# Performance work log

Hardware: AMD Instinct MI355X
Metric: run time of the kernel (lower is better)

The kernel has to match this reference:

```python
import jax, jax.numpy as jnp
import numpy as np

TEMP = 0.07  # temperature used as logits / 0.07 in the original


def setup_inputs() -> dict:
    key = jax.random.key(0)
    k1, k2, k3 = jax.random.split(key, 3)
    B, N, T, L, D = 8, 128, 8, 6, 256
    meta = jax.random.normal(k1, (B, N, T, L, D), dtype=jnp.float32)
    thing = jax.random.randint(k2, (B, N, T), 0, 2, dtype=jnp.int32)
    label = jax.random.randint(k3, (B, N, T), 0, 40, dtype=jnp.int32)
    return {"meta_weight_for_con": meta, "thing_gt_idx": thing, "label_tmp": label}


def _con_loss(meta, thing, label):
    # meta: [B,N,T,L,D]; thing,label: [B,N,T]
    B, N, T, L, D = meta.shape
    P = N * T
    valid = thing.reshape(B, P).astype(bool)            # [B,P] boolean gt mask
    lab = label.reshape(B, P)                           # [B,P]
    # meta_weight_b[mask] -> [K,L,D]; permute(1,0,2) -> per-layer [K,D].
    # We keep all P positions and mask instead of compacting (jit-friendly).
    w = meta.reshape(B, P, L, D).transpose(0, 2, 1, 3)  # [B,L,P,D]
    w = w / jnp.maximum(jnp.linalg.norm(w, axis=-1, keepdims=True), 1e-12)  # F.normalize
    z = jnp.einsum('blpd,blqd->blpq', w, w) / TEMP      # similarity / temp [B,L,P,P]

    same = lab[:, :, None] == lab[:, None, :]           # [B,P,P]
    vpair = valid[:, :, None] & valid[:, None, :]
    eye = jnp.eye(P, dtype=bool)
    pos_mask = same & (~eye) & vpair                    # positives: same label, not self
    neg_mask = (~same) & vpair                          # negatives: different label

    K = valid.sum(axis=1)                               # [B] ins_num_ per batch
    pos_count = pos_mask.sum(axis=-1)                   # [B,P]
    neg_count = neg_mask.sum(axis=-1)                   # [B,P]

    # --- random positive sample per (batch, layer, row), mirroring np.random.choice ---
    u = jax.random.uniform(jax.random.key(42), (B, L, P))
    r = jnp.floor(u * pos_count[:, None, :].astype(u.dtype)).astype(jnp.int32)
    r = jnp.minimum(r, jnp.maximum(pos_count - 1, 0)[:, None, :])
    ranks = jnp.cumsum(pos_mask, axis=-1) - 1           # rank of each positive in index order
    sel = pos_mask[:, None, :, :] & (ranks[:, None, :, :] == r[..., None])  # [B,L,P,P]
    zp = jnp.sum(jnp.where(sel, z, 0.0), axis=-1)       # chosen positive logit [B,L,P]
    diag = jnp.diagonal(z, axis1=-2, axis2=-1)          # self-sim fallback when no positives
    zp = jnp.where((pos_count > 0)[:, None, :], zp, diag)

    # --- last negative (original pads by repeating the last negative to K-1) ---
    iota = jnp.arange(P)
    idx_last = jnp.max(jnp.where(neg_mask, iota[None, None, :], -1), axis=-1)  # [B,P]
    idx = jnp.broadcast_to(jnp.maximum(idx_last, 0)[:, None, :, None], (B, L, P, 1))
    zl = jnp.take_along_axis(z, idx, axis=-1)[..., 0]   # [B,L,P]

    # --- stable CE with label 0: loss = lse(logits) - zp ---
    max_n = jnp.max(jnp.where(neg_mask[:, None], z, -jnp.inf), axis=-1)  # [B,L,P]
    m = jnp.maximum(zp, max_n)
    m = jnp.where(jnp.isfinite(m), m, zp)
    sum_neg = jnp.sum(jnp.where(neg_mask[:, None], jnp.exp(z - m[..., None]), 0.0), axis=-1)
    pad = jnp.maximum((K[:, None] - 1 - neg_count), 0).astype(z.dtype)   # [B,P]
    pad_term = pad[:, None, :] * jnp.where((neg_count > 0)[:, None, :], jnp.exp(zl - m), 0.0)
    loss_row = m + jnp.log(jnp.exp(zp - m) + sum_neg + pad_term) - zp    # [B,L,P]

    row_w = valid.astype(z.dtype)
    mean_per = jnp.sum(loss_row * row_w[:, None, :], axis=-1) / jnp.maximum(K, 1)[:, None].astype(z.dtype)  # [B,L]

    gate = jnp.sum((thing.sum(axis=2) > 0), axis=1) >= 2  # skip batches with <2 gt rows
    return jnp.sum(jnp.where(gate[:, None], mean_per, 0.0))


def reference(meta_weight_for_con, thing_gt_idx, label_tmp):
    return _con_loss(meta_weight_for_con, thing_gt_idx, label_tmp)
```

## Files before the change

### kernel.cpp

```cpp
#include <hip/hip_runtime.h>
#include <stdint.h>

namespace {

constexpr int Bb = 8, Ll = 6, Dd = 256, Pp = 1024;
constexpr float SCALE_Y = 14.285714285714286f * 1.4426950408889634f;
constexpr float M0y = 21.0f;
constexpr float LN2f = 0.6931471805599453f;

typedef __attribute__((ext_vector_type(4))) float floatx4;

__device__ const int PAIRS[36] = {
  0x00,0x01,0x02,0x03,0x04,0x05,0x06,0x07,
  0x11,0x12,0x13,0x14,0x15,0x16,0x17,
  0x22,0x23,0x24,0x25,0x26,0x27,
  0x33,0x34,0x35,0x36,0x37,
  0x44,0x45,0x46,0x47,
  0x55,0x56,0x57,
  0x66,0x67,
  0x77
};

__device__ __forceinline__ void async16(const void* g, void* l) {
  __builtin_amdgcn_global_load_lds(
      (const __attribute__((address_space(1))) void*)g,
      (__attribute__((address_space(3))) void*)l, 16, 0, 0);
}

__device__ __forceinline__ uint32_t rotl32(uint32_t x, int n) {
  return (x << n) | (x >> (32 - n));
}
__device__ __forceinline__ void tf_round(uint32_t& x0, uint32_t& x1, int r) {
  x0 += x1; x1 = rotl32(x1, r); x1 ^= x0;
}
__device__ void threefry2x32(uint32_t x0, uint32_t x1, uint32_t& o0, uint32_t& o1) {
  const uint32_t k0 = 0u, k1 = 42u;
  const uint32_t k2 = k0 ^ k1 ^ 0x1BD11BDAu;
  x0 += k0; x1 += k1;
  tf_round(x0,x1,13); tf_round(x0,x1,15); tf_round(x0,x1,26); tf_round(x0,x1,6);
  x0 += k1; x1 += k2 + 1u;
  tf_round(x0,x1,17); tf_round(x0,x1,29); tf_round(x0,x1,16); tf_round(x0,x1,24);
  x0 += k2; x1 += k0 + 2u;
  tf_round(x0,x1,13); tf_round(x0,x1,15); tf_round(x0,x1,26); tf_round(x0,x1,6);
  x0 += k0; x1 += k1 + 3u;
  tf_round(x0,x1,17); tf_round(x0,x1,29); tf_round(x0,x1,16); tf_round(x0,x1,24);
  x0 += k1; x1 += k2 + 4u;
  tf_round(x0,x1,13); tf_round(x0,x1,15); tf_round(x0,x1,26); tf_round(x0,x1,6);
  x0 += k2; x1 += k0 + 5u;
  o0 = x0; o1 = x1;
}
__device__ float jax_u01(uint32_t idx) {
  const uint32_t HALF = (uint32_t)(Bb * Ll * Pp / 2);
  uint32_t o0, o1, bits;
  if (idx < HALF) { threefry2x32(idx, idx + HALF, o0, o1); bits = o0; }
  else            { threefry2x32(idx - HALF, idx, o0, o1); bits = o1; }
  return __uint_as_float((bits >> 9) | 0x3f800000u) - 1.0f;
}

__device__ __forceinline__ uint32_t fp8e4m3_rne(float x) {
  uint32_t u = __float_as_uint(x);
  const uint32_t s = (u >> 24) & 0x80u;
  u &= 0x7FFFFFFFu;
  uint32_t code;
  if (u < 0x3C800000u) {
    code = (uint32_t)__float2int_rn(__uint_as_float(u) * 512.0f);
  } else {
    const uint32_t r = (u + 0x7FFFFu + ((u >> 20) & 1u)) >> 20;
    code = r - (120u << 3);
  }
  return s | code;
}
__device__ __forceinline__ float fp8e4m3_tof(uint32_t c) {
  const uint32_t e = (c >> 3) & 15u, m = c & 7u;
  float mag;
  if (e) mag = __uint_as_float(((e + 120u) << 23) | (m << 20));
  else   mag = (float)m * 0.001953125f;
  return (c & 0x80u) ? -mag : mag;
}

constexpr int NB_NORM = Bb * Pp * Ll / 4;
constexpr int NB_ROW  = Bb * Pp / 4;

__global__ void prep_k(const float* __restrict__ meta, const int* __restrict__ thing,
                       const int* __restrict__ label, uint8_t* __restrict__ wn,
                       int* __restrict__ qpos, int* __restrict__ negc,
                       int* __restrict__ qidx, int* __restrict__ Kv,
                       int* __restrict__ gatev, float* __restrict__ rowsum_g,
                       float* __restrict__ out) {
  __shared__ int sK[256], sG[256];
  const int bid = blockIdx.x, t = threadIdx.x;

  if (bid < NB_NORM) {
    const int wid = (bid * 256 + t) >> 6;
    const int lane = t & 63;
    const float4 v = *(const float4*)(meta + (size_t)wid * Dd + lane * 4);
    float ss = v.x * v.x + v.y * v.y + v.z * v.z + v.w * v.w;
    #pragma unroll
    for (int m = 32; m; m >>= 1) ss += __shfl_xor(ss, m, 64);
    const float inv = 1.0f / fmaxf(sqrtf(ss), 1e-12f);
    const int bp = wid / Ll, l = wid - bp * Ll;
    const int b = bp >> 10, p = bp & (Pp - 1);
    uint8_t* dst = wn + ((size_t)(b * Ll + l) * Pp + p) * Dd + lane * 4;
    const uint32_t packed = fp8e4m3_rne(v.x * inv)
                          | (fp8e4m3_rne(v.y * inv) << 8)
                          | (fp8e4m3_rne(v.z * inv) << 16)
                          | (fp8e4m3_rne(v.w * inv) << 24);
    *(uint32_t*)dst = packed;
    return;
  }
  if (bid < NB_NORM + NB_ROW) {
    const int wid = (bid - NB_NORM) * 4 + (t >> 6);
    const int lane = t & 63;
    const int b = wid >> 10, p = wid & (Pp - 1);
    const int* lab = label + b * Pp;
    const int* th  = thing + b * Pp;
    const int myLab = lab[p];
    const bool myValid = (th[p] != 0);

    uint32_t posbits = 0;
    int cnt[16];
    int pc = 0, nc = 0, last = -1;
    #pragma unroll
    for (int c = 0; c < 16; ++c) {
      const int q = c * 64 + lane;
      const int lq = lab[q];
      const bool vq = (th[q] != 0);
      const bool same = (lq == myLab);
      const bool pos = myValid && vq && same && (q != p);
      const bool neg = myValid && vq && !same;
      uint64_t bp2 = __ballot(pos);
      uint64_t bn = __ballot(neg);
      if (pos) posbits |= (1u << c);
      cnt[c] = __popcll(bp2);
      pc += cnt[c];
      nc += __popcll(bn);
      if (bn) last = c * 64 + 63 - __clzll(bn);
    }
    int qsel[Ll];
    #pragma unroll
    for (int l = 0; l < Ll; ++l) qsel[l] = p;
    if (pc > 0) {
      for (int l = 0; l < Ll; ++l) {
        const float u = jax_u01((uint32_t)((b * Ll + l) * Pp + p));
        int r = (int)floorf(u * (float)pc);
        r = min(r, pc - 1);
        int base = 0;
        for (int c = 0; c < 16; ++c) {
          if (r < base + cnt[c]) {
            const bool mine = (posbits >> c) & 1u;
            uint64_t bm = __ballot(mine);
            uint64_t ltmask = (lane == 0) ? 0ull : (~0ull >> (64 - lane));
            int myrank = __popcll(bm & ltmask);
            bool hit = mine && (base + myrank == r);
            uint64_t hb = __ballot(hit);
            qsel[l] = c * 64 + (int)__builtin_ctzll(hb);
            break;
          }
          base += cnt[c];
        }
      }
    }
    if (lane == 0) {
      negc[wid] = nc;
      qidx[wid] = (last < 0) ? 0 : last;
      #pragma unroll
      for (int l = 0; l < Ll; ++l) qpos[(b * Ll + l) * Pp + p] = qsel[l];
    }
    return;
  }
  if (bid < NB_NORM + NB_ROW + Bb) {
    const int b = bid - (NB_NORM + NB_ROW);
    int k = 0;
    for (int p = t; p < Pp; p += 256) k += (thing[b * Pp + p] != 0);
    int g = 0;
    if (t < 128) {
      int any = 0;
      for (int tt = 0; tt < 8; ++tt) any |= (thing[(b * 128 + t) * 8 + tt] != 0);
      g = any;
    }
    sK[t] = k; sG[t] = g;
    __syncthreads();
    for (int s = 128; s; s >>= 1) {
      if (t < s) { sK[t] += sK[t + s]; sG[t] += sG[t + s]; }
      __syncthreads();
    }
    if (t == 0) { Kv[b] = sK[0]; gatev[b] = (sG[0] >= 2) ? 1 : 0; }
    return;
  }
  if (bid < NB_NORM + NB_ROW + Bb + 48) {
    const int idx = (bid - (NB_NORM + NB_ROW + Bb)) * 256 + t;
    *(float4*)(rowsum_g + idx * 4) = (float4){0.f, 0.f, 0.f, 0.f};
    return;
  }
  if (t == 0) out[0] = 0.f;
}

__global__ void zpzl_k(const uint8_t* __restrict__ wn,
                       const int* __restrict__ qpos, const int* __restrict__ qidx,
                       float* __restrict__ zp_g, float* __restrict__ zl_g) {
  const int wid = blockIdx.x * 4 + (threadIdx.x >> 6);
  const int lane = threadIdx.x & 63;
  const int bl = wid >> 10, p = wid & (Pp - 1);
  const int b = bl / Ll;
  const int qp = qpos[bl * Pp + p];
  const int qi = qidx[b * Pp + p];
  const uint8_t* W = wn + (size_t)bl * Pp * Dd;
  const uint32_t a4 = *(const uint32_t*)(W + (size_t)p  * Dd + lane * 4);
  const uint32_t b4 = *(const uint32_t*)(W + (size_t)qp * Dd + lane * 4);
  const uint32_t c4 = *(const uint32_t*)(W + (size_t)qi * Dd + lane * 4);
  float sp = 0.f, sl = 0.f;
  #pragma unroll
  for (int i = 0; i < 4; ++i) {
    const float a = fp8e4m3_tof((a4 >> (8 * i)) & 0xFF);
    sp += a * fp8e4m3_tof((b4 >> (8 * i)) & 0xFF);
    sl += a * fp8e4m3_tof((c4 >> (8 * i)) & 0xFF);
  }
  #pragma unroll
  for (int m = 32; m; m >>= 1) {
    sp += __shfl_xor(sp, m, 64);
    sl += __shfl_xor(sl, m, 64);
  }
  if (lane == 0) {
    zp_g[bl * Pp + p] = sp * SCALE_Y;
    zl_g[bl * Pp + p] = sl * SCALE_Y;
  }
}

__global__ __launch_bounds__(256)
void gemm_loss_k(const uint8_t* __restrict__ wn,
                 const int* __restrict__ thing, const int* __restrict__ label,
                 float* __restrict__ rowsum_g) {
  __shared__ __align__(16) uint8_t As[128 * 128];
  __shared__ __align__(16) uint8_t Bs[128 * 128];
  __shared__ int labp_s[128], valp_s[128], labq_s[128], valq_s[128];
  __shared__ float rowsum_lds[128], colsum_lds[128];

  const int t = threadIdx.x;
  const int bid = blockIdx.x;
  const int xcd = bid & 7;
  const int chunk = bid >> 3;
  const int bl = xcd + 8 * (chunk % 6);
  const int b = bl / Ll;
  const int pair = PAIRS[chunk / 6];
  const int pt = pair >> 4, qt = pair & 15;
  const bool diag = (pt == qt);
  const int p0 = pt * 128, q0 = qt * 128;

  if (t < 128) {
    labp_s[t] = label[b * Pp + p0 + t];
    valp_s[t] = thing[b * Pp + p0 + t];
    labq_s[t] = label[b * Pp + q0 + t];
    valq_s[t] = thing[b * Pp + q0 + t];
    rowsum_lds[t] = 0.f;
    colsum_lds[t] = 0.f;
  }

  const uint8_t* Wbl = wn + (size_t)bl * Pp * Dd;
  const int lane = t & 63;
  const int w = t >> 6, wr = w >> 1, wc = w & 1;
  const int cq = lane & 15, rq = lane >> 4;
  const int wbase16 = (t & ~63) * 16;

  floatx4 acc[4][4];
  #pragma unroll
  for (int i = 0; i < 4; ++i)
    #pragma unroll
    for (int j = 0; j < 4; ++j) acc[i][j] = (floatx4){0.f, 0.f, 0.f, 0.f};

  const uint8_t* Bbase = diag ? As : Bs;

  for (int k0 = 0; k0 < Dd; k0 += 128) {
    __syncthreads();
    #pragma unroll
    for (int it = 0; it < 4; ++it) {
      const int c = it * 256 + t;
      const int row = c >> 3, sp = c & 7;
      const int sl = sp ^ (row & 7);
      async16(Wbl + (size_t)(p0 + row) * Dd + k0 + sl * 16, As + it * 4096 + wbase16);
      if (!diag)
        async16(Wbl + (size_t)(q0 + row) * Dd + k0 + sl * 16, Bs + it * 4096 + wbase16);
    }
    __syncthreads();
    #pragma unroll
    for (int sub = 0; sub < 4; ++sub) {
      const int Lw = sub * 2 + (rq >> 1);
      const int off8 = (rq & 1) * 8;
      long long af[4], bf[4];
      #pragma unroll
      for (int fi = 0; fi < 4; ++fi) {
        const int row = wr * 64 + fi * 16 + cq;
        af[fi] = *(const long long*)(As + row * 128 + (Lw ^ (row & 7)) * 16 + off8);
      }
      #pragma unroll
      for (int fj = 0; fj < 4; ++fj) {
        const int row = wc * 64 + fj * 16 + cq;
        bf[fj] = *(const long long*)(Bbase + row * 128 + (Lw ^ (row & 7)) * 16 + off8);
      }
      #pragma unroll
      for (int fi = 0; fi < 4; ++fi)
        #pragma unroll
        for (int fj = 0; fj < 4; ++fj)
          acc[fi][fj] = __builtin_amdgcn_mfma_f32_16x16x32_fp8_fp8(af[fi], bf[fj],
                                                                   acc[fi][fj], 0, 0, 0);
    }
  }

  int qlabv[4];
  float qvalf[4];
  float csum[4] = {0.f, 0.f, 0.f, 0.f};
  #pragma unroll
  for (int fj = 0; fj < 4; ++fj) {
    const int cl = wc * 64 + fj * 16 + cq;
    qlabv[fj] = labq_s[cl];
    qvalf[fj] = valq_s[cl] ? 1.f : 0.f;
  }
  #pragma unroll
  for (int fi = 0; fi < 4; ++fi) {
    #pragma unroll
    for (int reg = 0; reg < 4; ++reg) {
      const int rl = wr * 64 + fi * 16 + rq * 4 + reg;
      const int rlab = labp_s[rl];
      const float rvalf = valp_s[rl] ? 1.f : 0.f;
      float rsum = 0.f;
      #pragma unroll
      for (int fj = 0; fj < 4; ++fj) {
        const float y = acc[fi][fj][reg] * SCALE_Y;
        const float negm = (qlabv[fj] != rlab) ? (qvalf[fj] * rvalf) : 0.f;
        const float term = negm * exp2f(y - M0y);
        rsum += term;
        csum[fj] += term;
      }
      rsum += __shfl_xor(rsum, 1); rsum += __shfl_xor(rsum, 2);
      rsum += __shfl_xor(rsum, 4); rsum += __shfl_xor(rsum, 8);
      if (cq == 0) atomicAdd(&rowsum_lds[rl], rsum);
    }
  }
  if (!diag) {
    #pragma unroll
    for (int fj = 0; fj < 4; ++fj) {
      float c = csum[fj];
      c += __shfl_xor(c, 16); c += __shfl_xor(c, 32);
      if (rq == 0) atomicAdd(&colsum_lds[wc * 64 + fj * 16 + cq], c);
    }
  }
  __syncthreads();
  if (t < 128) {
    atomicAdd(&rowsum_g[bl * Pp + p0 + t], rowsum_lds[t]);
    if (!diag) atomicAdd(&rowsum_g[bl * Pp + q0 + t], colsum_lds[t]);
  }
}

__global__ void finalize_k(const float* __restrict__ rowsum_g, const float* __restrict__ zp_g,
                           const float* __restrict__ zl_g, const int* __restrict__ negc,
                           const int* __restrict__ thing, const int* __restrict__ Kv,
                           const int* __restrict__ gatev, float* __restrict__ out) {
  const int bl = blockIdx.x, b = bl / Ll, t = threadIdx.x;
  const int Kb = Kv[b];
  const float invK = 1.f / (float)max(Kb, 1);
  float acc = 0.f;
  for (int p = t; p < Pp; p += 256) {
    if (thing[b * Pp + p] != 0) {
      const float yp = zp_g[bl * Pp + p], yl = zl_g[bl * Pp + p];
      const float rs = rowsum_g[bl * Pp + p];
      const int nc = negc[b * Pp + p];
      const float pad = fmaxf((float)(Kb - 1 - nc), 0.f);
      const float tot = exp2f(yp - M0y) + rs + ((nc > 0) ? pad * exp2f(yl - M0y) : 0.f);
      acc += LN2f * (M0y + log2f(tot) - yp) * invK;
    }
  }
  __shared__ float sb[256];
  sb[t] = acc;
  __syncthreads();
  for (int s = 128; s; s >>= 1) {
    if (t < s) sb[t] += sb[t + s];
    __syncthreads();
  }
  if (t == 0 && gatev[b]) atomicAdd(out, sb[0]);
}

}

extern "C" void kernel_launch(void* const* d_in, const int* in_sizes, int n_in,
                              void* d_out, int out_size, void* d_ws, size_t ws_size,
                              hipStream_t stream) {
  const float* meta = (const float*)d_in[0];
  const int* thing  = (const int*)d_in[1];
  const int* label  = (const int*)d_in[2];
  float* out = (float*)d_out;

  char* ws = (char*)d_ws;
  size_t off = 0;
  uint8_t* wn = (uint8_t*)(ws + off); off += (size_t)Bb * Ll * Pp * Dd;
  int* qpos  = (int*)(ws + off); off += (size_t)Bb * Ll * Pp * 4;
  int* negc  = (int*)(ws + off); off += (size_t)Bb * Pp * 4;
  int* qidx  = (int*)(ws + off); off += (size_t)Bb * Pp * 4;
  int* Kv    = (int*)(ws + off); off += 64;
  int* gatev = (int*)(ws + off); off += 64;
  float* rowsum_g = (float*)(ws + off); off += (size_t)Bb * Ll * Pp * 4;
  float* zp_g     = (float*)(ws + off); off += (size_t)Bb * Ll * Pp * 4;
  float* zl_g     = (float*)(ws + off); off += (size_t)Bb * Ll * Pp * 4;

  const int nb_prep = NB_NORM + NB_ROW + Bb + 48 + 1;
  prep_k<<<nb_prep, 256, 0, stream>>>(meta, thing, label, wn, qpos, negc, qidx,
                                      Kv, gatev, rowsum_g, out);
  zpzl_k<<<(Bb * Ll * Pp) / 4, 256, 0, stream>>>(wn, qpos, qidx, zp_g, zl_g);
  gemm_loss_k<<<1728, 256, 0, stream>>>(wn, thing, label, rowsum_g);
  finalize_k<<<Bb * Ll, 256, 0, stream>>>(rowsum_g, zp_g, zl_g, negc, thing, Kv, gatev, out);
}
```

Baseline: 155.8 us.

## Fuse finalize into GEMM via last-block counter and load full K tile at once

The finalize kernel is removed. Its per-(b,l) loss reduction now runs inside the GEMM kernel, in whichever block is last to finish for that slice, detected with an atomic counter that prep_k zeroes. The GEMM also loads the whole 256-wide K dimension into LDS in one pass instead of two 128-wide passes, which removes a sync/reload round. The cost is doubled LDS use (64KB per block), which may lower occupancy, plus threadfence and atomic overhead at the end of each block.

```diff
diff --git a/kernel.cpp b/kernel.cpp
--- a/kernel.cpp
+++ b/kernel.cpp
@@ -86,7 +86,7 @@
                        int* __restrict__ qpos, int* __restrict__ negc,
                        int* __restrict__ qidx, int* __restrict__ Kv,
                        int* __restrict__ gatev, float* __restrict__ rowsum_g,
-                       float* __restrict__ out) {
+                       int* __restrict__ cnt, float* __restrict__ out) {
   __shared__ int sK[256], sG[256];
   const int bid = blockIdx.x, t = threadIdx.x;
 
@@ -118,7 +118,7 @@
     const bool myValid = (th[p] != 0);
 
     uint32_t posbits = 0;
-    int cnt[16];
+    int cntc[16];
     int pc = 0, nc = 0, last = -1;
     #pragma unroll
     for (int c = 0; c < 16; ++c) {
@@ -131,8 +131,8 @@
       uint64_t bp2 = __ballot(pos);
       uint64_t bn = __ballot(neg);
       if (pos) posbits |= (1u << c);
-      cnt[c] = __popcll(bp2);
-      pc += cnt[c];
+      cntc[c] = __popcll(bp2);
+      pc += cntc[c];
       nc += __popcll(bn);
       if (bn) last = c * 64 + 63 - __clzll(bn);
     }
@@ -146,7 +146,7 @@
         r = min(r, pc - 1);
         int base = 0;
         for (int c = 0; c < 16; ++c) {
-          if (r < base + cnt[c]) {
+          if (r < base + cntc[c]) {
             const bool mine = (posbits >> c) & 1u;
             uint64_t bm = __ballot(mine);
             uint64_t ltmask = (lane == 0) ? 0ull : (~0ull >> (64 - lane));
@@ -156,7 +156,7 @@
             qsel[l] = c * 64 + (int)__builtin_ctzll(hb);
             break;
           }
-          base += cnt[c];
+          base += cntc[c];
         }
       }
     }
@@ -193,6 +193,7 @@
     return;
   }
   if (t == 0) out[0] = 0.f;
+  if (t < 48) cnt[t] = 0;
 }
 
 __global__ void zpzl_k(const uint8_t* __restrict__ wn,
@@ -229,11 +230,15 @@
 __global__ __launch_bounds__(256)
 void gemm_loss_k(const uint8_t* __restrict__ wn,
                  const int* __restrict__ thing, const int* __restrict__ label,
-                 float* __restrict__ rowsum_g) {
-  __shared__ __align__(16) uint8_t As[128 * 128];
-  __shared__ __align__(16) uint8_t Bs[128 * 128];
+                 float* __restrict__ rowsum_g, const float* __restrict__ zp_g,
+                 const float* __restrict__ zl_g, const int* __restrict__ negc,
+                 const int* __restrict__ Kv, const int* __restrict__ gatev,
+                 int* __restrict__ cnt, float* __restrict__ out) {
+  __shared__ __align__(16) uint8_t As[128 * 256];
+  __shared__ __align__(16) uint8_t Bs[128 * 256];
   __shared__ int labp_s[128], valp_s[128], labq_s[128], valq_s[128];
   __shared__ float rowsum_lds[128], colsum_lds[128];
+  __shared__ int last_s;
 
   const int t = threadIdx.x;
   const int bid = blockIdx.x;
@@ -261,48 +266,46 @@
   const int cq = lane & 15, rq = lane >> 4;
   const int wbase16 = (t & ~63) * 16;
 
+  #pragma unroll
+  for (int it = 0; it < 8; ++it) {
+    const int c = it * 256 + t;
+    const int row = c >> 4, sp = c & 15;
+    const int sl = sp ^ (row & 15);
+    async16(Wbl + (size_t)(p0 + row) * Dd + sl * 16, As + it * 4096 + wbase16);
+    if (!diag)
+      async16(Wbl + (size_t)(q0 + row) * Dd + sl * 16, Bs + it * 4096 + wbase16);
+  }
+  __syncthreads();
+
+  const uint8_t* Bbase = diag ? As : Bs;
+
   floatx4 acc[4][4];
   #pragma unroll
   for (int i = 0; i < 4; ++i)
     #pragma unroll
     for (int j = 0; j < 4; ++j) acc[i][j] = (floatx4){0.f, 0.f, 0.f, 0.f};
 
-  const uint8_t* Bbase = diag ? As : Bs;
-
-  for (int k0 = 0; k0 < Dd; k0 += 128) {
-    __syncthreads();
-    #pragma unroll
-    for (int it = 0; it < 4; ++it) {
-      const int c = it * 256 + t;
-      const int row = c >> 3, sp = c & 7;
-      const int sl = sp ^ (row & 7);
-      async16(Wbl + (size_t)(p0 + row) * Dd + k0 + sl * 16, As + it * 4096 + wbase16);
-      if (!diag)
-        async16(Wbl + (size_t)(q0 + row) * Dd + k0 + sl * 16, Bs + it * 4096 + wbase16);
-    }
-    __syncthreads();
-    #pragma unroll
-    for (int sub = 0; sub < 4; ++sub) {
-      const int Lw = sub * 2 + (rq >> 1);
-      const int off8 = (rq & 1) * 8;
-      long long af[4], bf[4];
+  #pragma unroll
+  for (int sub = 0; sub < 8; ++sub) {
+    const int Lw = sub * 2 + (rq >> 1);
+    const int off8 = (rq & 1) * 8;
+    long long af[4], bf[4];
+    #pragma unroll
+    for (int fi = 0; fi < 4; ++fi) {
+      const int row = wr * 64 + fi * 16 + cq;
+      af[fi] = *(const long long*)(As + row * 256 + ((Lw ^ (row & 15)) << 4) + off8);
+    }
+    #pragma unroll
+    for (int fj = 0; fj < 4; ++fj) {
+      const int row = wc * 64 + fj * 16 + cq;
+      bf[fj] = *(const long long*)(Bbase + row * 256 + ((Lw ^ (row & 15)) << 4) + off8);
+    }
+    #pragma unroll
+    for (int fi = 0; fi < 4; ++fi)
       #pragma unroll
-      for (int fi = 0; fi < 4; ++fi) {
-        const int row = wr * 64 + fi * 16 + cq;
-        af[fi] = *(const long long*)(As + row * 128 + (Lw ^ (row & 7)) * 16 + off8);
-      }
-      #pragma unroll
-      for (int fj = 0; fj < 4; ++fj) {
-        const int row = wc * 64 + fj * 16 + cq;
-        bf[fj] = *(const long long*)(Bbase + row * 128 + (Lw ^ (row & 7)) * 16 + off8);
-      }
-      #pragma unroll
-      for (int fi = 0; fi < 4; ++fi)
-        #pragma unroll
-        for (int fj = 0; fj < 4; ++fj)
-          acc[fi][fj] = __builtin_amdgcn_mfma_f32_16x16x32_fp8_fp8(af[fi], bf[fj],
-                                                                   acc[fi][fj], 0, 0, 0);
-    }
+      for (int fj = 0; fj < 4; ++fj)
+        acc[fi][fj] = __builtin_amdgcn_mfma_f32_16x16x32_fp8_fp8(af[fi], bf[fj],
+                                                                 acc[fi][fj], 0, 0, 0);
   }
 
   int qlabv[4];
@@ -348,34 +351,35 @@
     atomicAdd(&rowsum_g[bl * Pp + p0 + t], rowsum_lds[t]);
     if (!diag) atomicAdd(&rowsum_g[bl * Pp + q0 + t], colsum_lds[t]);
   }
-}
-
-__global__ void finalize_k(const float* __restrict__ rowsum_g, const float* __restrict__ zp_g,
-                           const float* __restrict__ zl_g, const int* __restrict__ negc,
-                           const int* __restrict__ thing, const int* __restrict__ Kv,
-                           const int* __restrict__ gatev, float* __restrict__ out) {
-  const int bl = blockIdx.x, b = bl / Ll, t = threadIdx.x;
-  const int Kb = Kv[b];
-  const float invK = 1.f / (float)max(Kb, 1);
-  float acc = 0.f;
-  for (int p = t; p < Pp; p += 256) {
-    if (thing[b * Pp + p] != 0) {
-      const float yp = zp_g[bl * Pp + p], yl = zl_g[bl * Pp + p];
-      const float rs = rowsum_g[bl * Pp + p];
-      const int nc = negc[b * Pp + p];
-      const float pad = fmaxf((float)(Kb - 1 - nc), 0.f);
-      const float tot = exp2f(yp - M0y) + rs + ((nc > 0) ? pad * exp2f(yl - M0y) : 0.f);
-      acc += LN2f * (M0y + log2f(tot) - yp) * invK;
-    }
-  }
-  __shared__ float sb[256];
-  sb[t] = acc;
   __syncthreads();
-  for (int s = 128; s; s >>= 1) {
-    if (t < s) sb[t] += sb[t + s];
+  if (t == 0) {
+    __threadfence();
+    last_s = (atomicAdd(&cnt[bl], 1) == 35);
+  }
+  __syncthreads();
+
+  if (last_s) {
+    __threadfence();
+    const int Kb = Kv[b];
+    const float invK = 1.f / (float)max(Kb, 1);
+    float acc2 = 0.f;
+    for (int p = t; p < Pp; p += 256) {
+      if (thing[b * Pp + p] != 0) {
+        const float yp = zp_g[bl * Pp + p], yl = zl_g[bl * Pp + p];
+        const float rs = rowsum_g[bl * Pp + p];
+        const int nc = negc[b * Pp + p];
+        const float pad = fmaxf((float)(Kb - 1 - nc), 0.f);
+        const float tot = exp2f(yp - M0y) + rs + ((nc > 0) ? pad * exp2f(yl - M0y) : 0.f);
+        acc2 += LN2f * (M0y + log2f(tot) - yp) * invK;
+      }
+    }
+    #pragma unroll
+    for (int m = 32; m; m >>= 1) acc2 += __shfl_xor(acc2, m, 64);
+    if (lane == 0) colsum_lds[w] = acc2;
     __syncthreads();
-  }
-  if (t == 0 && gatev[b]) atomicAdd(out, sb[0]);
+    if (t == 0 && gatev[b])
+      atomicAdd(out, colsum_lds[0] + colsum_lds[1] + colsum_lds[2] + colsum_lds[3]);
+  }
 }
 
 }
@@ -396,14 +400,15 @@
   int* qidx  = (int*)(ws + off); off += (size_t)Bb * Pp * 4;
   int* Kv    = (int*)(ws + off); off += 64;
   int* gatev = (int*)(ws + off); off += 64;
+  int* cnt   = (int*)(ws + off); off += 64 * 4;
   float* rowsum_g = (float*)(ws + off); off += (size_t)Bb * Ll * Pp * 4;
   float* zp_g     = (float*)(ws + off); off += (size_t)Bb * Ll * Pp * 4;
   float* zl_g     = (float*)(ws + off); off += (size_t)Bb * Ll * Pp * 4;
 
   const int nb_prep = NB_NORM + NB_ROW + Bb + 48 + 1;
   prep_k<<<nb_prep, 256, 0, stream>>>(meta, thing, label, wn, qpos, negc, qidx,
-                                      Kv, gatev, rowsum_g, out);
+                                      Kv, gatev, rowsum_g, cnt, out);
   zpzl_k<<<(Bb * Ll * Pp) / 4, 256, 0, stream>>>(wn, qpos, qidx, zp_g, zl_g);
-  gemm_loss_k<<<1728, 256, 0, stream>>>(wn, thing, label, rowsum_g);
-  finalize_k<<<Bb * Ll, 256, 0, stream>>>(rowsum_g, zp_g, zl_g, negc, thing, Kv, gatev, out);
-}
+  gemm_loss_k<<<1728, 256, 0, stream>>>(wn, thing, label, rowsum_g, zp_g, zl_g,
+                                        negc, Kv, gatev, cnt, out);
+}
```

Result: slower. 175.5 us (+12.6%).
